# Performance work log

Measured on AMD Instinct MI355X. Metric: run time of the kernel, lower is better.

## Reference

```python
import jax, jax.numpy as jnp
import numpy as np

B, S, E, H = 16, 512, 4096, 8
HD = E // H  # 512, must equal S for this module's math
LN_EPS = 1e-5
NORM_EPS = 1e-12


def setup_inputs() -> dict:
    key = jax.random.key(0)
    ks = jax.random.split(key, 16)
    s_e = 1.0 / np.sqrt(E)
    s_h = 1.0 / np.sqrt(HD)
    return {
        "x": jax.random.normal(ks[0], (B, S, E), jnp.float32),
        "Wq": jax.random.normal(ks[1], (E, E), jnp.float32) * s_e,
        "bq": jnp.zeros((E,), jnp.float32),
        "Wk": jax.random.normal(ks[2], (E, E), jnp.float32) * s_e,
        "bk": jnp.zeros((E,), jnp.float32),
        "Wv": jax.random.normal(ks[3], (E, E), jnp.float32) * s_e,
        "bv": jnp.zeros((E,), jnp.float32),
        "g_q": jnp.ones((HD,), jnp.float32),
        "b_q": jnp.zeros((HD,), jnp.float32),
        "g_k": jnp.ones((HD,), jnp.float32),
        "b_k": jnp.zeros((HD,), jnp.float32),
        "Wg": jax.random.normal(ks[4], (2 * HD, HD), jnp.float32) * s_h,
        "bg": jnp.zeros((2 * HD,), jnp.float32),
        "Wo": jax.random.normal(ks[5], (E, E), jnp.float32) * s_e,
        "bo": jnp.zeros((E,), jnp.float32),
    }


def _layernorm(t, g, b):
    mu = jnp.mean(t, axis=-1, keepdims=True)
    var = jnp.mean(jnp.square(t - mu), axis=-1, keepdims=True)
    return (t - mu) * jax.lax.rsqrt(var + LN_EPS) * g + b


def reference(x, Wq, bq, Wk, bk, Wv, bv, g_q, b_q, g_k, b_k, Wg, bg, Wo, bo):
    # projections + head split: [B,H,S,HD]
    def proj(W, bias):
        y = jnp.einsum('bse,fe->bsf', x, W) + bias
        return y.reshape(B, S, H, HD).transpose(0, 2, 1, 3)

    q = proj(Wq, bq)
    k = proj(Wk, bk)
    v = proj(Wv, bv)

    # per-head QK LayerNorm over head_dim
    q = _layernorm(q, g_q, b_q)
    k = _layernorm(k, g_k, b_k)

    # scores [B,H,S,S]; note S == HD by construction
    scores = jnp.einsum('bhsd,bhtd->bhst', q, k) / np.sqrt(HD)

    # GeGLU over last dim (linear HD -> 2*HD, chunk, gelu gate)
    h = jnp.einsum('bhst,ft->bhsf', scores, Wg) + bg
    val, gate = h[..., :HD], h[..., HD:]
    w = val * jax.nn.gelu(gate, approximate=False)

    # L2 normalize over last dim (torch F.normalize p=2)
    norm = jnp.sqrt(jnp.sum(jnp.square(w), axis=-1, keepdims=True))
    w = w / jnp.maximum(norm, NORM_EPS)

    # attention-value matmul: [B,H,S,HD] x [B,H,S,HD] with HD==S
    out = jnp.einsum('bhst,bhtd->bhsd', w, v)
    out = out.transpose(0, 2, 1, 3).reshape(B, S, E)
    return jnp.einsum('bse,fe->bsf', out, Wo) + bo
```

## Files before the change

### kernel.cpp

```cpp
#include <hip/hip_runtime.h>
#include <math.h>

typedef __bf16 bf16x8 __attribute__((ext_vector_type(8)));
typedef float f32x4 __attribute__((ext_vector_type(4)));
typedef short short8 __attribute__((ext_vector_type(8)));
typedef unsigned int uint4v __attribute__((ext_vector_type(4)));

__device__ __forceinline__ float bf2f(unsigned short u) {
  union { unsigned int i; float f; } v; v.i = ((unsigned int)u) << 16; return v.f;
}
__device__ __forceinline__ unsigned short f2bf(float f) {
  union { float fl; unsigned int i; } v; v.fl = f;
  unsigned int x = v.i;
  return (unsigned short)((x + 0x7FFFu + ((x >> 16) & 1u)) >> 16);
}
__device__ __forceinline__ unsigned int cvt_pk_bf16(float lo, float hi) {
  unsigned int r;
  asm("v_cvt_pk_bf16_f32 %0, %1, %2" : "=v"(r) : "v"(lo), "v"(hi));
  return r;
}
__device__ __forceinline__ void gl_lds16(const unsigned short* g, void* l) {
  __builtin_amdgcn_global_load_lds(
      (const __attribute__((address_space(1))) unsigned int*)g,
      (__attribute__((address_space(3))) unsigned int*)l, 16, 0, 0);
}

template<int BATCH, int SPLIT3, int CF32, int HAS_BIAS>
__global__ __launch_bounds__(512)
void gemm256(const unsigned short* __restrict__ A,
             const unsigned short* __restrict__ B,
             const float* __restrict__ b0, const float* __restrict__ b1,
             const float* __restrict__ b2,
             void* __restrict__ C0, void* __restrict__ C1, void* __restrict__ C2,
             int K, int lda, int ldb, int ldc, int nbn, float alpha,
             long sAo, long sAi, int nAi,
             long sBo, long sBi, int nBi,
             long sCo, long sCi, int nCi)
{
  __shared__ alignas(16) unsigned char LDS[131072];
  const int NT = K >> 6;

  int tm, tn;
  long offA = 0, offB = 0, offC = 0;
  if (BATCH) {
    const int bx = (int)blockIdx.x;
    tm = (bx / nbn) * 256;
    tn = (bx % nbn) * 256;
    const int z = (int)blockIdx.z;
    offA = (long)(z / nAi) * sAo + (long)(z % nAi) * sAi;
    offB = (long)(z / nBi) * sBo + (long)(z % nBi) * sBi;
    offC = (long)(z / nCi) * sCo + (long)(z % nCi) * sCi;
  } else {
    const int nwg = (int)gridDim.x;
    const int bid = (int)blockIdx.x;
    const int s = (bid & 7) * (nwg >> 3) + (bid >> 3);
    const int sTile = s >> 4, w = s & 15;
    const int snb = nbn >> 2;
    tm = ((sTile / snb) * 4 + (w >> 2)) * 256;
    tn = ((sTile % snb) * 4 + (w & 3)) * 256;
  }

  const int tid = (int)threadIdx.x;
  const int lane = tid & 63;
  const int wv = tid >> 6;
  const int wm = wv >> 2;
  const int wn = wv & 3;
  const int l16 = lane & 15;
  const int kg = lane >> 4;

  const int srow = tid >> 3;
  const int scolb = ((tid & 7) * 16) ^ (((tid >> 3) & 7) << 4);
  const unsigned short* Abase = A + offA + (long)tm * lda + (scolb >> 1);
  const unsigned short* Bbase = B + offB + (long)tn * ldb + (scolb >> 1);
  const int ldsw = wv * 1024;

  const int colswz0 = (kg * 16) ^ ((l16 & 7) << 4);
  const int colswz1 = (64 + kg * 16) ^ ((l16 & 7) << 4);

  f32x4 acc[8][4];
  #pragma unroll
  for (int i = 0; i < 8; ++i)
    #pragma unroll
    for (int j = 0; j < 4; ++j)
      #pragma unroll
      for (int e = 0; e < 4; ++e) acc[i][j][e] = 0.f;

  auto stageAh = [&](int t, int h) {
    const int buf = t & 1;
    #pragma unroll
    for (int i = 0; i < 2; ++i)
      gl_lds16(Abase + (long)(h * 128 + srow + i * 64) * lda + t * 64,
               &LDS[buf * 32768 + h * 16384 + i * 8192 + ldsw]);
  };
  auto stageBh = [&](int t, int h) {
    const int buf = t & 1;
    #pragma unroll
    for (int i = 0; i < 2; ++i)
      gl_lds16(Bbase + (long)(h * 128 + srow + i * 64) * ldb + t * 64,
               &LDS[65536 + buf * 32768 + h * 16384 + i * 8192 + ldsw]);
  };

  stageAh(0, 0); stageAh(0, 1); stageBh(0, 0); stageBh(0, 1);
  stageAh(1, 0); stageAh(1, 1); stageBh(1, 0); stageBh(1, 1);
  asm volatile("s_waitcnt vmcnt(8)" ::: "memory");
  __builtin_amdgcn_s_barrier();

  for (int t = 0; t < NT; ++t) {
    const unsigned char* aB = &LDS[(t & 1) * 32768 + wm * 16384];
    const unsigned char* bB = &LDS[65536 + (t & 1) * 32768 + (wn >> 1) * 16384];
    const int brow = (wn & 1) * 64;
    bf16x8 bfrag[4][2];
    #pragma unroll
    for (int j = 0; j < 4; ++j) {
      bf16x8 a0k0 = *(const bf16x8*)(aB + ((2 * j + 0) * 16 + l16) * 128 + colswz0);
      bf16x8 a0k1 = *(const bf16x8*)(aB + ((2 * j + 0) * 16 + l16) * 128 + colswz1);
      bf16x8 a1k0 = *(const bf16x8*)(aB + ((2 * j + 1) * 16 + l16) * 128 + colswz0);
      bf16x8 a1k1 = *(const bf16x8*)(aB + ((2 * j + 1) * 16 + l16) * 128 + colswz1);
      if (j == 0) {
        #pragma unroll
        for (int ni = 0; ni < 4; ++ni) {
          bfrag[ni][0] = *(const bf16x8*)(bB + (brow + ni * 16 + l16) * 128 + colswz0);
          bfrag[ni][1] = *(const bf16x8*)(bB + (brow + ni * 16 + l16) * 128 + colswz1);
        }
        if (t > 0 && t + 1 < NT) stageAh(t + 1, 0);
      } else if (j == 1) {
        if (t > 0 && t + 1 < NT) stageAh(t + 1, 1);
      } else if (j == 2) {
        if (t + 2 < NT) stageBh(t + 2, 0);
      } else {
        if (t + 2 < NT) stageBh(t + 2, 1);
      }
      asm volatile("s_waitcnt lgkmcnt(0)" ::: "memory");
      __builtin_amdgcn_sched_barrier(0);
      __builtin_amdgcn_s_setprio(1);
      #pragma unroll
      for (int ni = 0; ni < 4; ++ni) {
        acc[2 * j + 0][ni] = __builtin_amdgcn_mfma_f32_16x16x32_bf16(a0k0, bfrag[ni][0], acc[2 * j + 0][ni], 0, 0, 0);
        acc[2 * j + 0][ni] = __builtin_amdgcn_mfma_f32_16x16x32_bf16(a0k1, bfrag[ni][1], acc[2 * j + 0][ni], 0, 0, 0);
        acc[2 * j + 1][ni] = __builtin_amdgcn_mfma_f32_16x16x32_bf16(a1k0, bfrag[ni][0], acc[2 * j + 1][ni], 0, 0, 0);
        acc[2 * j + 1][ni] = __builtin_amdgcn_mfma_f32_16x16x32_bf16(a1k1, bfrag[ni][1], acc[2 * j + 1][ni], 0, 0, 0);
      }
      __builtin_amdgcn_s_setprio(0);
      if (j == 1) {
        __builtin_amdgcn_s_barrier();
      } else if (j == 3) {
        if (t >= NT - 2) { asm volatile("s_waitcnt vmcnt(0)" ::: "memory"); }
        else             { asm volatile("s_waitcnt vmcnt(4)" ::: "memory"); }
        __builtin_amdgcn_sched_barrier(0);
        __builtin_amdgcn_s_barrier();
      }
    }
  }

  const int which = SPLIT3 ? (tn >> 12) : 0;
  const float* bp = SPLIT3 ? (which == 0 ? b0 : (which == 1 ? b1 : b2)) : b0;
  void* Cp = SPLIT3 ? (which == 0 ? C0 : (which == 1 ? C1 : C2)) : C0;
  const int tnn = SPLIT3 ? (tn & 4095) : tn;

  if (CF32) {
    #pragma unroll
    for (int ni = 0; ni < 4; ++ni) {
      const int col = tnn + wn * 64 + ni * 16 + l16;
      const float bv = HAS_BIAS ? bp[col] : 0.f;
      #pragma unroll
      for (int mi = 0; mi < 8; ++mi)
        #pragma unroll
        for (int jj = 0; jj < 4; ++jj) {
          const int row = tm + wm * 128 + mi * 16 + kg * 4 + jj;
          ((float*)Cp)[offC + (long)row * ldc + col] = acc[mi][ni][jj] * alpha + bv;
        }
    }
  } else {
    unsigned short* lw = (unsigned short*)&LDS[wv * 16384];
    #pragma unroll
    for (int ni = 0; ni < 4; ++ni) {
      const float bv = HAS_BIAS ? bp[tnn + wn * 64 + ni * 16 + l16] : 0.f;
      #pragma unroll
      for (int mi = 0; mi < 8; ++mi)
        #pragma unroll
        for (int jj = 0; jj < 4; ++jj)
          lw[(mi * 16 + kg * 4 + jj) * 64 + ni * 16 + l16] =
              f2bf(acc[mi][ni][jj] * alpha + bv);
    }
    asm volatile("s_waitcnt lgkmcnt(0)" ::: "memory");
    __builtin_amdgcn_sched_barrier(0);
    unsigned short* Cg = (unsigned short*)Cp + offC +
                         (long)(tm + wm * 128) * ldc + tnn + wn * 64;
    const int rr = lane >> 3, cc = (lane & 7) * 8;
    #pragma unroll
    for (int i = 0; i < 16; ++i) {
      short8 val = *(const short8*)&lw[(i * 8 + rr) * 64 + cc];
      *(short8*)(Cg + (long)(i * 8 + rr) * ldc + cc) = val;
    }
  }
}

__global__ __launch_bounds__(256)
void cvt_bf16(const float* __restrict__ in, unsigned short* __restrict__ out, long n8)
{
  long i = (long)blockIdx.x * 256 + threadIdx.x;
  const long stride = (long)gridDim.x * 256;
  for (; i < n8; i += stride) {
    f32x4 v0 = *(const f32x4*)(in + i * 8);
    f32x4 v1 = *(const f32x4*)(in + i * 8 + 4);
    uint4v o;
    o[0] = cvt_pk_bf16(v0[0], v0[1]);
    o[1] = cvt_pk_bf16(v0[2], v0[3]);
    o[2] = cvt_pk_bf16(v1[0], v1[1]);
    o[3] = cvt_pk_bf16(v1[2], v1[3]);
    *(uint4v*)(out + i * 8) = o;
  }
}

__global__ __launch_bounds__(256)
void ln_rows(unsigned short* __restrict__ t, const float* __restrict__ g,
             const float* __restrict__ b)
{
  const int row = blockIdx.x * 4 + ((int)threadIdx.x >> 6);
  const int lane = (int)threadIdx.x & 63;
  unsigned short* p = t + (long)row * 512 + lane * 8;
  short8 rv = *(const short8*)p;
  float x[8];
  #pragma unroll
  for (int j = 0; j < 8; ++j) x[j] = bf2f((unsigned short)rv[j]);
  float s = 0.f;
  #pragma unroll
  for (int j = 0; j < 8; ++j) s += x[j];
  #pragma unroll
  for (int off = 32; off > 0; off >>= 1) s += __shfl_xor(s, off, 64);
  float mu = s * (1.f / 512.f);
  float vs = 0.f;
  #pragma unroll
  for (int j = 0; j < 8; ++j) { float d = x[j] - mu; vs += d * d; }
  #pragma unroll
  for (int off = 32; off > 0; off >>= 1) vs += __shfl_xor(vs, off, 64);
  float rs = rsqrtf(vs * (1.f / 512.f) + 1e-5f);
  f32x4 gv0 = *(const f32x4*)(g + lane * 8);
  f32x4 gv1 = *(const f32x4*)(g + lane * 8 + 4);
  f32x4 bv0 = *(const f32x4*)(b + lane * 8);
  f32x4 bv1 = *(const f32x4*)(b + lane * 8 + 4);
  short8 ov;
  #pragma unroll
  for (int j = 0; j < 4; ++j) ov[j] = (short)f2bf((x[j] - mu) * rs * gv0[j] + bv0[j]);
  #pragma unroll
  for (int j = 0; j < 4; ++j) ov[4 + j] = (short)f2bf((x[4 + j] - mu) * rs * gv1[j] + bv1[j]);
  *(short8*)p = ov;
}

__global__ __launch_bounds__(256)
void gate_norm(const unsigned short* __restrict__ h, unsigned short* __restrict__ w)
{
  const int row = blockIdx.x * 4 + ((int)threadIdx.x >> 6);
  const int lane = (int)threadIdx.x & 63;
  const unsigned short* hp = h + (long)row * 1024 + lane * 8;
  short8 vv = *(const short8*)hp;
  short8 gg = *(const short8*)(hp + 512);
  float wv[8];
  float ssq = 0.f;
  #pragma unroll
  for (int j = 0; j < 8; ++j) {
    float val = bf2f((unsigned short)vv[j]);
    float gt  = bf2f((unsigned short)gg[j]);
    float tt  = val * (0.5f * gt * (1.f + erff(gt * 0.70710678118654752f)));
    wv[j] = tt;
    ssq += tt * tt;
  }
  #pragma unroll
  for (int off = 32; off > 0; off >>= 1) ssq += __shfl_xor(ssq, off, 64);
  float scale = 1.f / fmaxf(sqrtf(ssq), 1e-12f);
  short8 ov;
  #pragma unroll
  for (int j = 0; j < 8; ++j) ov[j] = (short)f2bf(wv[j] * scale);
  *(short8*)(w + (long)row * 512 + lane * 8) = ov;
}

__global__ __launch_bounds__(256)
void transpose_v(const unsigned short* __restrict__ v, unsigned short* __restrict__ vT)
{
  __shared__ alignas(16) unsigned short lt[64][72];
  const int bh = blockIdx.z;
  const int b = bh >> 3, hh = bh & 7;
  const int d0 = blockIdx.x * 64, t0 = blockIdx.y * 64;
  const int tid = (int)threadIdx.x;
  const unsigned short* src = v + (long)b * (512L * 4096L) + hh * 512;
  #pragma unroll
  for (int it = 0; it < 2; ++it) {
    int ci = it * 256 + tid;
    int r = ci >> 3, c8 = (ci & 7) * 8;
    *(short8*)&lt[r][c8] = *(const short8*)(src + (long)(t0 + r) * 4096 + d0 + c8);
  }
  __syncthreads();
  unsigned short* dst = vT + ((long)bh * 512 + d0) * 512 + t0;
  #pragma unroll
  for (int it = 0; it < 2; ++it) {
    int ci = it * 256 + tid;
    int rr = ci >> 3, c8 = (ci & 7) * 8;
    short8 o;
    #pragma unroll
    for (int j = 0; j < 8; ++j) o[j] = (short)lt[c8 + j][rr];
    *(short8*)(dst + (long)rr * 512 + c8) = o;
  }
}

extern "C" void kernel_launch(void* const* d_in, const int* in_sizes, int n_in,
                              void* d_out, int out_size, void* d_ws, size_t ws_size,
                              hipStream_t stream)
{
  (void)in_sizes; (void)n_in; (void)out_size; (void)ws_size;
  const float* x   = (const float*)d_in[0];
  const float* Wq  = (const float*)d_in[1];
  const float* bq  = (const float*)d_in[2];
  const float* Wk  = (const float*)d_in[3];
  const float* bk  = (const float*)d_in[4];
  const float* Wv  = (const float*)d_in[5];
  const float* bv  = (const float*)d_in[6];
  const float* g_q = (const float*)d_in[7];
  const float* b_q = (const float*)d_in[8];
  const float* g_k = (const float*)d_in[9];
  const float* b_k = (const float*)d_in[10];
  const float* Wg  = (const float*)d_in[11];
  const float* bg  = (const float*)d_in[12];
  const float* Wo  = (const float*)d_in[13];
  const float* bo  = (const float*)d_in[14];
  float* out = (float*)d_out;

  const long NE  = 33554432L;
  const long NE2 = NE / 2;
  unsigned short* ws    = (unsigned short*)d_ws;
  unsigned short* xb    = ws;
  unsigned short* Wqkv  = ws + NE;
  unsigned short* qbuf  = ws + NE + 3 * NE2;
  unsigned short* kbuf  = qbuf + NE;
  unsigned short* vbuf  = kbuf + NE;
  unsigned short* Wgb   = Wqkv;
  unsigned short* Wob   = Wqkv + 524288;
  unsigned short* sbuf  = xb;
  unsigned short* vT    = qbuf;
  unsigned short* hbuf  = kbuf;
  unsigned short* wbuf  = xb;
  unsigned short* obuf  = kbuf;

  dim3 blk256(256), blk512(512);
  const float isq = 0.044194173824159216f;

  cvt_bf16<<<16384, blk256, 0, stream>>>(x, xb, NE / 8);
  cvt_bf16<<<8192, blk256, 0, stream>>>(Wq, Wqkv, NE2 / 8);
  cvt_bf16<<<8192, blk256, 0, stream>>>(Wk, Wqkv + NE2, NE2 / 8);
  cvt_bf16<<<8192, blk256, 0, stream>>>(Wv, Wqkv + 2 * NE2, NE2 / 8);

  gemm256<0, 1, 0, 1><<<1536, blk512, 0, stream>>>(
      xb, Wqkv, bq, bk, bv, qbuf, kbuf, vbuf,
      4096, 4096, 4096, 4096, 48, 1.f,
      0L, 0L, 1, 0L, 0L, 1, 0L, 0L, 1);

  cvt_bf16<<<256, blk256, 0, stream>>>(Wg, Wgb, 524288L / 8);
  cvt_bf16<<<8192, blk256, 0, stream>>>(Wo, Wob, NE2 / 8);

  ln_rows<<<16384, blk256, 0, stream>>>(qbuf, g_q, b_q);
  ln_rows<<<16384, blk256, 0, stream>>>(kbuf, g_k, b_k);

  gemm256<1, 0, 0, 0><<<dim3(4, 1, 128), blk512, 0, stream>>>(
      qbuf, kbuf, nullptr, nullptr, nullptr, sbuf, nullptr, nullptr,
      512, 4096, 4096, 512, 2, isq,
      2097152L, 512L, 8,
      2097152L, 512L, 8,
      262144L, 0L, 1);

  transpose_v<<<dim3(8, 8, 128), blk256, 0, stream>>>(vbuf, vT);

  gemm256<1, 0, 0, 1><<<dim3(8, 1, 128), blk512, 0, stream>>>(
      sbuf, Wgb, bg, nullptr, nullptr, hbuf, nullptr, nullptr,
      512, 512, 512, 1024, 4, 1.f,
      262144L, 0L, 1,
      0L, 0L, 1,
      524288L, 0L, 1);

  gate_norm<<<16384, blk256, 0, stream>>>(hbuf, wbuf);

  gemm256<1, 0, 0, 0><<<dim3(4, 1, 128), blk512, 0, stream>>>(
      wbuf, vT, nullptr, nullptr, nullptr, obuf, nullptr, nullptr,
      512, 512, 512, 4096, 2, 1.f,
      262144L, 0L, 1,
      262144L, 0L, 1,
      2097152L, 512L, 8);

  gemm256<0, 0, 1, 1><<<512, blk512, 0, stream>>>(
      obuf, Wob, bo, nullptr, nullptr, out, nullptr, nullptr,
      4096, 4096, 4096, 4096, 16, 1.f,
      0L, 0L, 1, 0L, 0L, 1, 0L, 0L, 1);
}
```

Before: 1.296 ms.

## Fuse V transpose into QKV GEMM epilogue and merge conversion/layernorm launches

The QKV projection GEMM now writes the V third directly in transposed per-head layout through a swizzled LDS staging buffer, which removes the separate transpose_v kernel and its extra read and write of V. The four fp32→bf16 conversions and the two weight conversions are each merged into a single multi-source launch, and the q/k layernorms into one launch. The fp32 output and transposed-V stores now use nontemporal stores. Buffer aliasing is reshuffled so hbuf reuses qbuf and vT lives in the old vbuf slot.

```diff
diff --git a/kernel.cpp b/kernel.cpp
--- a/kernel.cpp
+++ b/kernel.cpp
@@ -167,8 +167,37 @@
         #pragma unroll
         for (int jj = 0; jj < 4; ++jj) {
           const int row = tm + wm * 128 + mi * 16 + kg * 4 + jj;
-          ((float*)Cp)[offC + (long)row * ldc + col] = acc[mi][ni][jj] * alpha + bv;
+          __builtin_nontemporal_store(acc[mi][ni][jj] * alpha + bv,
+                                      &((float*)Cp)[offC + (long)row * ldc + col]);
         }
+    }
+  } else if (SPLIT3 && which == 2) {
+    unsigned short* lw = (unsigned short*)&LDS[wv * 16384];
+    #pragma unroll
+    for (int ni = 0; ni < 4; ++ni) {
+      const int dl = ni * 16 + l16;
+      const float bv = HAS_BIAS ? bp[tnn + wn * 64 + dl] : 0.f;
+      #pragma unroll
+      for (int mi = 0; mi < 8; ++mi)
+        #pragma unroll
+        for (int jj = 0; jj < 4; ++jj) {
+          const int tl = mi * 16 + kg * 4 + jj;
+          lw[dl * 128 + (tl ^ ((dl & 7) << 4))] = f2bf(acc[mi][ni][jj] * alpha + bv);
+        }
+    }
+    asm volatile("s_waitcnt lgkmcnt(0)" ::: "memory");
+    __builtin_amdgcn_sched_barrier(0);
+    const int b = tm >> 9, hh = tnn >> 9;
+    const int dbase = (tnn & 511) + wn * 64;
+    const int tbase = (tm & 511) + wm * 128;
+    unsigned short* vTg = (unsigned short*)C2 +
+                          ((long)(b * 8 + hh) * 512 + dbase) * 512 + tbase;
+    const int dr = lane >> 4, t8 = (lane & 15) * 8;
+    #pragma unroll
+    for (int i = 0; i < 16; ++i) {
+      const int dl = i * 4 + dr;
+      short8 val = *(const short8*)&lw[dl * 128 + (t8 ^ ((dl & 7) << 4))];
+      __builtin_nontemporal_store(val, (short8*)(vTg + (long)dl * 512 + t8));
     }
   } else {
     unsigned short* lw = (unsigned short*)&LDS[wv * 16384];
@@ -196,29 +225,45 @@
 }
 
 __global__ __launch_bounds__(256)
-void cvt_bf16(const float* __restrict__ in, unsigned short* __restrict__ out, long n8)
+void cvt_multi(const float* __restrict__ s0, long n0,
+               const float* __restrict__ s1, long n1,
+               const float* __restrict__ s2, long n2,
+               const float* __restrict__ s3, long n3,
+               unsigned short* __restrict__ dst, long n8)
 {
   long i = (long)blockIdx.x * 256 + threadIdx.x;
   const long stride = (long)gridDim.x * 256;
   for (; i < n8; i += stride) {
-    f32x4 v0 = *(const f32x4*)(in + i * 8);
-    f32x4 v1 = *(const f32x4*)(in + i * 8 + 4);
+    long e = i * 8;
+    const float* src;
+    if (e < n0)                    src = s0 + e;
+    else if (e < n0 + n1)          src = s1 + (e - n0);
+    else if (e < n0 + n1 + n2)     src = s2 + (e - n0 - n1);
+    else                           src = s3 + (e - n0 - n1 - n2);
+    f32x4 v0 = *(const f32x4*)(src);
+    f32x4 v1 = *(const f32x4*)(src + 4);
     uint4v o;
     o[0] = cvt_pk_bf16(v0[0], v0[1]);
     o[1] = cvt_pk_bf16(v0[2], v0[3]);
     o[2] = cvt_pk_bf16(v1[0], v1[1]);
     o[3] = cvt_pk_bf16(v1[2], v1[3]);
-    *(uint4v*)(out + i * 8) = o;
+    *(uint4v*)(dst + e) = o;
   }
 }
 
 __global__ __launch_bounds__(256)
-void ln_rows(unsigned short* __restrict__ t, const float* __restrict__ g,
-             const float* __restrict__ b)
+void ln_rows2(unsigned short* __restrict__ q, const float* __restrict__ gq,
+              const float* __restrict__ bq_, unsigned short* __restrict__ k,
+              const float* __restrict__ gk, const float* __restrict__ bk_,
+              int rows_per_tensor)
 {
-  const int row = blockIdx.x * 4 + ((int)threadIdx.x >> 6);
+  int row = blockIdx.x * 4 + ((int)threadIdx.x >> 6);
   const int lane = (int)threadIdx.x & 63;
-  unsigned short* p = t + (long)row * 512 + lane * 8;
+  unsigned short* base = q;
+  const float* g = gq;
+  const float* b = bq_;
+  if (row >= rows_per_tensor) { row -= rows_per_tensor; base = k; g = gk; b = bk_; }
+  unsigned short* p = base + (long)row * 512 + lane * 8;
   short8 rv = *(const short8*)p;
   float x[8];
   #pragma unroll
@@ -272,34 +317,6 @@
   #pragma unroll
   for (int j = 0; j < 8; ++j) ov[j] = (short)f2bf(wv[j] * scale);
   *(short8*)(w + (long)row * 512 + lane * 8) = ov;
-}
-
-__global__ __launch_bounds__(256)
-void transpose_v(const unsigned short* __restrict__ v, unsigned short* __restrict__ vT)
-{
-  __shared__ alignas(16) unsigned short lt[64][72];
-  const int bh = blockIdx.z;
-  const int b = bh >> 3, hh = bh & 7;
-  const int d0 = blockIdx.x * 64, t0 = blockIdx.y * 64;
-  const int tid = (int)threadIdx.x;
-  const unsigned short* src = v + (long)b * (512L * 4096L) + hh * 512;
-  #pragma unroll
-  for (int it = 0; it < 2; ++it) {
-    int ci = it * 256 + tid;
-    int r = ci >> 3, c8 = (ci & 7) * 8;
-    *(short8*)&lt[r][c8] = *(const short8*)(src + (long)(t0 + r) * 4096 + d0 + c8);
-  }
-  __syncthreads();
-  unsigned short* dst = vT + ((long)bh * 512 + d0) * 512 + t0;
-  #pragma unroll
-  for (int it = 0; it < 2; ++it) {
-    int ci = it * 256 + tid;
-    int rr = ci >> 3, c8 = (ci & 7) * 8;
-    short8 o;
-    #pragma unroll
-    for (int j = 0; j < 8; ++j) o[j] = (short)lt[c8 + j][rr];
-    *(short8*)(dst + (long)rr * 512 + c8) = o;
-  }
 }
 
 extern "C" void kernel_launch(void* const* d_in, const int* in_sizes, int n_in,
@@ -331,33 +348,30 @@
   unsigned short* Wqkv  = ws + NE;
   unsigned short* qbuf  = ws + NE + 3 * NE2;
   unsigned short* kbuf  = qbuf + NE;
-  unsigned short* vbuf  = kbuf + NE;
+  unsigned short* vT    = kbuf + NE;
   unsigned short* Wgb   = Wqkv;
   unsigned short* Wob   = Wqkv + 524288;
   unsigned short* sbuf  = xb;
-  unsigned short* vT    = qbuf;
-  unsigned short* hbuf  = kbuf;
+  unsigned short* hbuf  = qbuf;
   unsigned short* wbuf  = xb;
   unsigned short* obuf  = kbuf;
 
   dim3 blk256(256), blk512(512);
   const float isq = 0.044194173824159216f;
 
-  cvt_bf16<<<16384, blk256, 0, stream>>>(x, xb, NE / 8);
-  cvt_bf16<<<8192, blk256, 0, stream>>>(Wq, Wqkv, NE2 / 8);
-  cvt_bf16<<<8192, blk256, 0, stream>>>(Wk, Wqkv + NE2, NE2 / 8);
-  cvt_bf16<<<8192, blk256, 0, stream>>>(Wv, Wqkv + 2 * NE2, NE2 / 8);
+  cvt_multi<<<20480, blk256, 0, stream>>>(x, NE, Wq, NE2, Wk, NE2, Wv, NE2,
+                                          ws, (NE + 3 * NE2) / 8);
 
   gemm256<0, 1, 0, 1><<<1536, blk512, 0, stream>>>(
-      xb, Wqkv, bq, bk, bv, qbuf, kbuf, vbuf,
+      xb, Wqkv, bq, bk, bv, qbuf, kbuf, vT,
       4096, 4096, 4096, 4096, 48, 1.f,
       0L, 0L, 1, 0L, 0L, 1, 0L, 0L, 1);
 
-  cvt_bf16<<<256, blk256, 0, stream>>>(Wg, Wgb, 524288L / 8);
-  cvt_bf16<<<8192, blk256, 0, stream>>>(Wo, Wob, NE2 / 8);
-
-  ln_rows<<<16384, blk256, 0, stream>>>(qbuf, g_q, b_q);
-  ln_rows<<<16384, blk256, 0, stream>>>(kbuf, g_k, b_k);
+  cvt_multi<<<8192, blk256, 0, stream>>>(Wg, 524288L, Wo, NE2,
+                                         nullptr, 0L, nullptr, 0L,
+                                         Wgb, (524288L + NE2) / 8);
+
+  ln_rows2<<<32768, blk256, 0, stream>>>(qbuf, g_q, b_q, kbuf, g_k, b_k, 65536);
 
   gemm256<1, 0, 0, 0><<<dim3(4, 1, 128), blk512, 0, stream>>>(
       qbuf, kbuf, nullptr, nullptr, nullptr, sbuf, nullptr, nullptr,
@@ -366,8 +380,6 @@
       2097152L, 512L, 8,
       262144L, 0L, 1);
 
-  transpose_v<<<dim3(8, 8, 128), blk256, 0, stream>>>(vbuf, vT);
-
   gemm256<1, 0, 0, 1><<<dim3(8, 1, 128), blk512, 0, stream>>>(
       sbuf, Wgb, bg, nullptr, nullptr, hbuf, nullptr, nullptr,
       512, 512, 512, 1024, 4, 1.f,
```

Measured after the change: 1.235 ms. 4.7% less time.
